# Performance work log

Measured on AMD Instinct MI355X. Metric: run time of the kernel, lower is better.

The kernel has to match this reference:

```python
import jax, jax.numpy as jnp
import numpy as np

D = 1024
H = 16
HD = D // H
T = 2048
B = 2
EPS = 1e-7

def setup_inputs() -> dict:
    key = jax.random.key(0)
    ks = jax.random.split(key, 16)
    s = 0.02
    return {
        "x":  jax.random.normal(ks[0], (B, T, D), jnp.float32),
        "Wq": jax.random.normal(ks[1], (D, D), jnp.float32) * s,
        "bq": jnp.zeros((D,), jnp.float32),
        "Wk": jax.random.normal(ks[2], (D, D), jnp.float32) * s,
        "bk": jnp.zeros((D,), jnp.float32),
        "Wv": jax.random.normal(ks[3], (D, D), jnp.float32) * s,
        "bv": jnp.zeros((D,), jnp.float32),
        "Wo": jax.random.normal(ks[4], (D, D), jnp.float32) * s,
        "bo": jnp.zeros((D,), jnp.float32),
        "W1": jax.random.normal(ks[5], (D, 4 * D), jnp.float32) * s,
        "b1": jnp.zeros((4 * D,), jnp.float32),
        "W2": jax.random.normal(ks[6], (4 * D, D), jnp.float32) * s,
        "b2": jnp.zeros((D,), jnp.float32),
        "g1": jnp.ones((D,), jnp.float32),
        "be1": jnp.zeros((D,), jnp.float32),
        "g2": jnp.ones((D,), jnp.float32),
        "be2": jnp.zeros((D,), jnp.float32),
    }

def layer_norm(x, gamma, beta):
    mu = jnp.mean(x, axis=-1, keepdims=True)
    var = jnp.mean(jnp.square(x - mu), axis=-1, keepdims=True)  # biased var
    return (x - mu) / jnp.sqrt(var + EPS) * gamma + beta

def attention(x, Wq, bq, Wk, bk, Wv, bv, Wo, bo):
    b, t, d = x.shape
    q = (x @ Wq + bq).reshape(b, t, H, HD).transpose(0, 2, 1, 3)  # [B,H,T,HD]
    k = (x @ Wk + bk).reshape(b, t, H, HD).transpose(0, 2, 1, 3)
    v = (x @ Wv + bv).reshape(b, t, H, HD).transpose(0, 2, 1, 3)
    scores = jnp.einsum("bhqd,bhkd->bhqk", q, k) / np.sqrt(HD).astype(np.float32)
    causal = jnp.tril(jnp.ones((t, t), bool))
    scores = jnp.where(causal, scores, -jnp.inf)
    attn = jax.nn.softmax(scores, axis=-1)
    out = jnp.einsum("bhqk,bhkd->bhqd", attn, v)
    out = out.transpose(0, 2, 1, 3).reshape(b, t, d)
    return out @ Wo + bo

def reference(x, Wq, bq, Wk, bk, Wv, bv, Wo, bo, W1, b1, W2, b2, g1, be1, g2, be2):
    x = x + attention(layer_norm(x, g1, be1), Wq, bq, Wk, bk, Wv, bv, Wo, bo)
    h = layer_norm(x, g2, be2)
    x = x + (jax.nn.relu(h @ W1 + b1) @ W2 + b2)
    return x
```

## Files before the change

### kernel.cpp

```cpp
#include <hip/hip_runtime.h>
#include <hip/hip_bf16.h>

#define Dm 1024
#define Hn 16
#define HDm 64
#define Tm 2048
#define Bm 2
#define MR (Bm*Tm)
#define SQK 3072

typedef __attribute__((ext_vector_type(8))) short bfrag8;
typedef __attribute__((ext_vector_type(4))) float floatx4;

__device__ __forceinline__ float bf2f(ushort u){
  union { unsigned int i; float f; } c; c.i = ((unsigned int)u)<<16; return c.f;
}
__device__ __forceinline__ ushort f2bf(float f){
  unsigned int u = __float_as_uint(f);
  u += 0x7fffu + ((u>>16)&1u);
  return (ushort)(u>>16);
}
__device__ __forceinline__ void gl2lds16(const ushort* g, ushort* l){
  __builtin_amdgcn_global_load_lds(
    (const __attribute__((address_space(1))) unsigned int*)g,
    (__attribute__((address_space(3))) unsigned int*)l,
    16, 0, 0);
}
__device__ __forceinline__ int is_f32(const unsigned int* g1w){
  return *g1w == 0x3F800000u;
}

__global__ __launch_bounds__(256) void prep_vec(const void* bq, const void* bk, const void* bv,
                                                const void* bo, const void* b1, const void* b2,
                                                const void* g1, const void* be1,
                                                const void* g2, const void* be2,
                                                float* __restrict__ dst){
  int i = blockIdx.x*256 + threadIdx.x;
  if (i >= 13312) return;
  int f = is_f32((const unsigned int*)g1);
  const void* src; int off;
  if      (i < 1024)  { src = bq;  off = i; }
  else if (i < 2048)  { src = bk;  off = i-1024; }
  else if (i < 3072)  { src = bv;  off = i-2048; }
  else if (i < 4096)  { src = bo;  off = i-3072; }
  else if (i < 8192)  { src = b1;  off = i-4096; }
  else if (i < 9216)  { src = b2;  off = i-8192; }
  else if (i < 10240) { src = g1;  off = i-9216; }
  else if (i < 11264) { src = be1; off = i-10240; }
  else if (i < 12288) { src = g2;  off = i-11264; }
  else                { src = be2; off = i-12288; }
  dst[i] = f ? ((const float*)src)[off] : bf2f(((const ushort*)src)[off]);
}

__device__ __forceinline__ void transpose_body(const void* src, ushort* dst,
                                               int K, int N, int f32){
  __shared__ ushort s[32][33];
  int bx = blockIdx.x, by = blockIdx.y;
  int tx = threadIdx.x, ty = threadIdx.y;
#pragma unroll
  for(int r=0;r<4;r++){
    size_t gi = (size_t)(by*32+ty+8*r)*N + bx*32+tx;
    s[ty+8*r][tx] = f32 ? f2bf(((const float*)src)[gi]) : ((const ushort*)src)[gi];
  }
  __syncthreads();
#pragma unroll
  for(int r=0;r<4;r++)
    dst[(size_t)(bx*32+ty+8*r)*K + by*32+tx] = s[tx][ty+8*r];
}
__global__ __launch_bounds__(256) void transpose_cast(const void* __restrict__ src,
                                                      ushort* __restrict__ dst,
                                                      int K, int N, const unsigned int* g1w){
  transpose_body(src, dst, K, N, is_f32(g1w));
}
__global__ __launch_bounds__(256) void transpose_qkvo(const void* Wq, const void* Wk,
                                                      const void* Wv, const void* Wo,
                                                      ushort* __restrict__ Wqkvt,
                                                      ushort* __restrict__ Wot,
                                                      const unsigned int* g1w){
  int z = blockIdx.z;
  const void* src = (z==0)?Wq:(z==1)?Wk:(z==2)?Wv:Wo;
  ushort* dst = (z<3) ? (Wqkvt + (size_t)z*1024*1024) : Wot;
  transpose_body(src, dst, 1024, 1024, is_f32(g1w));
}

__global__ __launch_bounds__(256) void vtrans(const ushort* __restrict__ qkv,
                                              ushort* __restrict__ vt){
  __shared__ ushort s[32][33];
  int bhz = blockIdx.z;
  int bx = blockIdx.x;
  int by = blockIdx.y;
  int tx = threadIdx.x, ty = threadIdx.y;
  int b = bhz>>4, h = bhz&15;
  const ushort* src = qkv + (size_t)b*Tm*SQK + 2048 + h*64;
#pragma unroll
  for(int r=0;r<4;r++)
    s[ty+8*r][tx] = src[(size_t)(bx*32+ty+8*r)*SQK + by*32+tx];
  __syncthreads();
  ushort* dst = vt + (size_t)bhz*HDm*Tm;
#pragma unroll
  for(int r=0;r<4;r++)
    dst[(size_t)(by*32+ty+8*r)*Tm + bx*32+tx] = s[tx][ty+8*r];
}

template<int MODE>
__global__ __launch_bounds__(256) void ln_kernel(const void* __restrict__ xin,
                                                 const float* __restrict__ g,
                                                 const float* __restrict__ be,
                                                 ushort* __restrict__ out,
                                                 const unsigned int* g1w){
  int row = blockIdx.x;
  int tid = threadIdx.x;
  size_t base = (size_t)row*Dm + tid*4;
  float v[4];
  bool f32in = (MODE==1) || (MODE==0 && is_f32(g1w));
  if (f32in){
    const float4 t = *(const float4*)((const float*)xin + base);
    v[0]=t.x; v[1]=t.y; v[2]=t.z; v[3]=t.w;
  } else {
    ushort4 t = *(const ushort4*)((const ushort*)xin + base);
    v[0]=bf2f(t.x); v[1]=bf2f(t.y); v[2]=bf2f(t.z); v[3]=bf2f(t.w);
  }
  float s  = v[0]+v[1]+v[2]+v[3];
  float s2 = v[0]*v[0]+v[1]*v[1]+v[2]*v[2]+v[3]*v[3];
#pragma unroll
  for(int o=1;o<64;o<<=1){
    s  += __shfl_xor(s,  o, 64);
    s2 += __shfl_xor(s2, o, 64);
  }
  __shared__ float red[8];
  int wv = tid>>6;
  if ((tid&63)==0){ red[wv]=s; red[wv+4]=s2; }
  __syncthreads();
  s  = red[0]+red[1]+red[2]+red[3];
  s2 = red[4]+red[5]+red[6]+red[7];
  float mu  = s  * (1.0f/Dm);
  float var = s2 * (1.0f/Dm) - mu*mu;
  float rstd = rsqrtf(var + 1e-7f);
  float4 gg = *(const float4*)(g  + tid*4);
  float4 bb = *(const float4*)(be + tid*4);
  ushort4 o4;
  o4.x = f2bf((v[0]-mu)*rstd*gg.x+bb.x);
  o4.y = f2bf((v[1]-mu)*rstd*gg.y+bb.y);
  o4.z = f2bf((v[2]-mu)*rstd*gg.z+bb.z);
  o4.w = f2bf((v[3]-mu)*rstd*gg.w+bb.w);
  *(ushort4*)(out + base) = o4;
}

#define BKt 64
enum { E_BF16=0, E_RELU=1, E_OPROJ=2, E_FINALB=3, E_PARTB=4 };

template<int EPI>
__global__ __launch_bounds__(256) void gemm_bt(const ushort* __restrict__ A, int lda,
                                               const ushort* __restrict__ Bt, int ldb,
                                               const float* __restrict__ bias,
                                               void* __restrict__ Cout, int ldc,
                                               int Ki,
                                               const unsigned int* g1w){
  __shared__ ushort As[128*BKt];
  __shared__ ushort Bs[128*BKt];
  int tid = threadIdx.x;
  int bn = blockIdx.x, bm = blockIdx.y;
  int wv = tid>>6, lane = tid&63;
  int quad = lane>>4, l16 = lane&15;
  int wm = (wv&1)*64, wn = (wv>>1)*64;
  floatx4 acc[4][4] = {};
  int koff = (EPI==E_PARTB) ? blockIdx.z*Ki : 0;
  const ushort* Aptr = A  + (size_t)bm*128*lda + koff;
  const ushort* Bptr = Bt + (size_t)bn*128*ldb + koff;
  int rl = lane>>3;
  int cs = ((lane&7) ^ rl)*8;

  for(int k0=0; k0<Ki; k0+=BKt){
    __syncthreads();
#pragma unroll
    for(int c=0;c<4;c++){
      gl2lds16(&Aptr[(size_t)(wv*32 + c*8 + rl)*lda + k0 + cs], &As[(wv*32 + c*8)*BKt]);
      gl2lds16(&Bptr[(size_t)(wv*32 + c*8 + rl)*ldb + k0 + cs], &Bs[(wv*32 + c*8)*BKt]);
    }
    __syncthreads();
#pragma unroll
    for(int f=0;f<2;f++){
      int sw = (((f<<2)|quad) ^ (l16&7))*8;
      bfrag8 a[4], b[4];
#pragma unroll
      for(int i=0;i<4;i++) a[i] = *(const bfrag8*)&As[(wm+i*16+l16)*BKt + sw];
#pragma unroll
      for(int j=0;j<4;j++) b[j] = *(const bfrag8*)&Bs[(wn+j*16+l16)*BKt + sw];
#pragma unroll
      for(int i=0;i<4;i++)
#pragma unroll
        for(int j=0;j<4;j++)
          acc[i][j] = __builtin_amdgcn_mfma_f32_16x16x32_bf16(a[i], b[j], acc[i][j], 0,0,0);
    }
  }

  ushort* part = (EPI==E_PARTB) ? ((ushort*)Cout + (size_t)blockIdx.z*MR*1024) : (ushort*)Cout;
#pragma unroll
  for(int i=0;i<4;i++){
    int gr = bm*128 + wm + i*16 + quad*4;
#pragma unroll
    for(int j=0;j<4;j++){
      int gc = bn*128 + wn + j*16 + l16;
      float bb = (EPI==E_PARTB) ? 0.0f : bias[gc];
#pragma unroll
      for(int rg=0; rg<4; rg++){
        size_t idx = (size_t)(gr+rg)*ldc + gc;
        float val = acc[i][j][rg] + bb;
        if (EPI==E_BF16)        part[idx] = f2bf(val);
        else if (EPI==E_RELU)   part[idx] = f2bf(val>0.0f?val:0.0f);
        else       part[idx] = f2bf(val);
      }
    }
  }
}

__global__ __launch_bounds__(256) void ffn2_reduce(const ushort* __restrict__ p0,
                                                   const ushort* __restrict__ p1,
                                                   const float* __restrict__ bias,
                                                   const ushort* __restrict__ resid,
                                                   void* __restrict__ out,
                                                   const unsigned int* g1w){
  int e = (blockIdx.x*256 + threadIdx.x)*4;
  ushort4 a = *(const ushort4*)&p0[e];
  ushort4 b = *(const ushort4*)&p1[e];
  ushort4 r = *(const ushort4*)&resid[e];
  float4 bb = *(const float4*)&bias[e & 1023];
  float v0 = bf2f(a.x)+bf2f(b.x)+bb.x+bf2f(r.x);
  float v1 = bf2f(a.y)+bf2f(b.y)+bb.y+bf2f(r.y);
  float v2 = bf2f(a.z)+bf2f(b.z)+bb.z+bf2f(r.z);
  float v3 = bf2f(a.w)+bf2f(b.w)+bb.w+bf2f(r.w);
  if (is_f32(g1w)){
    float4 o = {v0,v1,v2,v3};
    *(float4*)((float*)out + e) = o;
  } else {
    ushort4 o = {f2bf(v0),f2bf(v1),f2bf(v2),f2bf(v3)};
    *(ushort4*)((ushort*)out + e) = o;
  }
}

template<int EPI>
__global__ __launch_bounds__(128) void gemm64_bt(const ushort* __restrict__ A, int lda,
                                                 const ushort* __restrict__ Bt, int ldb,
                                                 const float* __restrict__ bias,
                                                 const void*   __restrict__ resid,
                                                 void* __restrict__ Cout, int ldc,
                                                 int Ki,
                                                 const unsigned int* g1w){
  __shared__ ushort As[64*BKt];
  __shared__ ushort Bs[64*BKt];
  int tid = threadIdx.x;
  int id = blockIdx.x;
  int xcd = id&7, sdec = id>>3;
  int bn = sdec&15, bm = (sdec>>4)*8 + xcd;
  int wv = tid>>6, lane = tid&63;
  int quad = lane>>4, l16 = lane&15;
  int wm = wv*32;
  floatx4 acc[2][4] = {};
  const ushort* Aptr = A  + (size_t)bm*64*lda;
  const ushort* Bptr = Bt + (size_t)bn*64*ldb;
  int rl = lane>>3;
  int cs = ((lane&7) ^ rl)*8;

  for(int k0=0; k0<Ki; k0+=BKt){
    __syncthreads();
#pragma unroll
    for(int c=0;c<4;c++){
      gl2lds16(&Aptr[(size_t)(wv*32 + c*8 + rl)*lda + k0 + cs], &As[(wv*32 + c*8)*BKt]);
      gl2lds16(&Bptr[(size_t)(wv*32 + c*8 + rl)*ldb + k0 + cs], &Bs[(wv*32 + c*8)*BKt]);
    }
    __syncthreads();
#pragma unroll
    for(int f=0;f<2;f++){
      int sw = (((f<<2)|quad) ^ (l16&7))*8;
      bfrag8 a[2], b[4];
#pragma unroll
      for(int i=0;i<2;i++) a[i] = *(const bfrag8*)&As[(wm+i*16+l16)*BKt + sw];
#pragma unroll
      for(int j=0;j<4;j++) b[j] = *(const bfrag8*)&Bs[(j*16+l16)*BKt + sw];
#pragma unroll
      for(int i=0;i<2;i++)
#pragma unroll
        for(int j=0;j<4;j++)
          acc[i][j] = __builtin_amdgcn_mfma_f32_16x16x32_bf16(a[i], b[j], acc[i][j], 0,0,0);
    }
  }

  int f32 = is_f32(g1w);
#pragma unroll
  for(int i=0;i<2;i++){
    int gr = bm*64 + wm + i*16 + quad*4;
#pragma unroll
    for(int j=0;j<4;j++){
      int gc = bn*64 + j*16 + l16;
      float bb = bias[gc];
#pragma unroll
      for(int rg=0; rg<4; rg++){
        size_t idx = (size_t)(gr+rg)*ldc + gc;
        float val = acc[i][j][rg] + bb;
        if (EPI==E_OPROJ){
          float r = f32 ? ((const float*)resid)[idx] : bf2f(((const ushort*)resid)[idx]);
          ((ushort*)Cout)[idx] = f2bf(val + r);
        } else {
          float r = bf2f(((const ushort*)resid)[idx]);
          if (f32) ((float*)Cout)[idx] = val + r;
          else     ((ushort*)Cout)[idx] = f2bf(val + r);
        }
      }
    }
  }
}

#define PSTR2 136

__global__ __launch_bounds__(256) void attn_mfma(const ushort* __restrict__ qkv,
                                                 const ushort* __restrict__ vt,
                                                 ushort* __restrict__ out){
  __shared__ ushort Ks[128*64];
  __shared__ ushort Vs[64*128];
  __shared__ ushort Ps[64*PSTR2];
  int id = blockIdx.x;
  int xcd = id&7, sdec = id>>3;
  int bxp = sdec&15, hb = sdec>>4;
  int h = xcd + 8*(hb&1), b = hb>>1;
  int tid = threadIdx.x;
  int wv = tid>>6, lane = tid&63;
  int quad = lane>>4, l16 = lane&15;
  const ushort* qbase = qkv + (size_t)b*Tm*SQK + h*HDm;
  const ushort* kbase = qbase + Dm;
  const ushort* vtb   = vt + (size_t)(b*Hn+h)*HDm*Tm;
  size_t obase = (size_t)b*Tm*Dm + (size_t)h*HDm;
  int rl = lane>>3;
  int cs = ((lane&7) ^ rl)*8;
  int vrow = lane>>4;
  int l7 = l16 & 7;

  for(int half=0; half<2; half++){
    int qt = half ? (31 - bxp) : bxp;
    int qrow = qt*64 + wv*16 + l16;
    bfrag8 aq[2];
#pragma unroll
    for(int f=0;f<2;f++){
      bfrag8 raw = *(const bfrag8*)&qbase[(size_t)qrow*SQK + f*32 + quad*8];
#pragma unroll
      for(int e=0;e<8;e++) aq[f][e] = (short)f2bf(bf2f((ushort)raw[e])*0.125f);
    }

    floatx4 oacc[4] = {};
    float lacc[4] = {0.0f,0.0f,0.0f,0.0f};
    int qabs0 = qt*64 + wv*16 + quad*4;
    int nr = (qt+2)>>1;

    for(int r=0; r<nr; r++){
      __syncthreads();
#pragma unroll
      for(int c=0;c<4;c++){
        int kr0 = wv*32 + c*8;
        gl2lds16(&kbase[(size_t)(r*128 + kr0 + rl)*SQK + cs], &Ks[kr0*64]);
        int d0 = wv*16 + c*4;
        int drow = d0 + vrow;
        int gg = (lane&15) ^ (drow&7);
        gl2lds16(&vtb[(size_t)drow*Tm + r*128 + gg*8], &Vs[d0*128]);
      }
      __syncthreads();

      floatx4 s[8];
#pragma unroll
      for(int j=0;j<8;j++){
        int kr = j*16 + l16;
        int k7 = kr & 7;
        bfrag8 b0 = *(const bfrag8*)&Ks[kr*64 + ((quad     ^ k7)*8)];
        bfrag8 b1 = *(const bfrag8*)&Ks[kr*64 + (((4|quad) ^ k7)*8)];
        floatx4 z = {0.0f,0.0f,0.0f,0.0f};
        z = __builtin_amdgcn_mfma_f32_16x16x32_bf16(aq[0], b0, z, 0,0,0);
        z = __builtin_amdgcn_mfma_f32_16x16x32_bf16(aq[1], b1, z, 0,0,0);
        s[j] = z;
      }
      if (2*r+1 >= qt){
#pragma unroll
        for(int j=0;j<8;j++){
          int gk = r*128 + j*16 + l16;
#pragma unroll
          for(int rg=0;rg<4;rg++)
            if (gk > qabs0 + rg) s[j][rg] = -1.0e30f;
        }
      }

#pragma unroll
      for(int j=0;j<8;j++)
#pragma unroll
        for(int rg=0;rg<4;rg++){
          float p = __expf(s[j][rg]);
          lacc[rg] += p;
          Ps[(wv*16 + quad*4+rg)*PSTR2 + j*16 + l16] = f2bf(p);
        }

      bfrag8 ap[4];
#pragma unroll
      for(int c=0;c<4;c++)
        ap[c] = *(const bfrag8*)&Ps[(wv*16 + l16)*PSTR2 + (c*4+quad)*8];
#pragma unroll
      for(int j=0;j<4;j++){
        int dr = j*16 + l16;
        int d7 = dr & 7;
#pragma unroll
        for(int c=0;c<4;c++){
          bfrag8 bv = *(const bfrag8*)&Vs[dr*128 + (((c*4+quad) ^ d7)*8)];
          oacc[j] = __builtin_amdgcn_mfma_f32_16x16x32_bf16(ap[c], bv, oacc[j], 0,0,0);
        }
      }
    }

#pragma unroll
    for(int o=1;o<16;o<<=1)
#pragma unroll
      for(int rg=0;rg<4;rg++) lacc[rg] += __shfl_xor(lacc[rg], o, 64);
    float inv[4];
#pragma unroll
    for(int rg=0;rg<4;rg++) inv[rg] = 1.0f / lacc[rg];

#pragma unroll
    for(int j=0;j<4;j++)
#pragma unroll
      for(int rg=0;rg<4;rg++){
        int t = qt*64 + wv*16 + quad*4 + rg;
        out[obase + (size_t)t*Dm + j*16 + l16] = f2bf(oacc[j][rg] * inv[rg]);
      }
  }
}

extern "C" void kernel_launch(void* const* d_in, const int* in_sizes, int n_in,
                              void* d_out, int out_size, void* d_ws, size_t ws_size,
                              hipStream_t stream) {
  const void* x   = d_in[0];
  const void* Wq  = d_in[1];
  const void* bq  = d_in[2];
  const void* Wk  = d_in[3];
  const void* bk  = d_in[4];
  const void* Wv  = d_in[5];
  const void* bv  = d_in[6];
  const void* Wo  = d_in[7];
  const void* bo  = d_in[8];
  const void* W1  = d_in[9];
  const void* b1  = d_in[10];
  const void* W2  = d_in[11];
  const void* b2  = d_in[12];
  const void* g1  = d_in[13];
  const void* be1 = d_in[14];
  const void* g2  = d_in[15];
  const void* be2 = d_in[16];
  const unsigned int* g1w = (const unsigned int*)g1;

  char* ws = (char*)d_ws;
  const size_t MB = 1024*1024;
  float*  biasf = (float*)(ws + 65536);
  ushort* Wqkvt = (ushort*)(ws + 1*MB);
  ushort* Wot   = (ushort*)(ws + 7*MB);
  ushort* W1t   = (ushort*)(ws + 9*MB);
  ushort* W2t   = (ushort*)(ws + 17*MB);
  ushort* p0    = (ushort*)(ws + 1*MB);
  ushort* p1    = (ushort*)(ws + 9*MB);
  ushort* ln1   = (ushort*)(ws + 25*MB);
  ushort* vtb   = (ushort*)(ws + 25*MB);
  ushort* h2    = (ushort*)(ws + 25*MB);
  ushort* qkv   = (ushort*)(ws + 33*MB);
  ushort* atb   = (ushort*)(ws + 57*MB);
  ushort* x1b   = (ushort*)(ws + 65*MB);
  ushort* h1    = (ushort*)(ws + 33*MB);

  prep_vec<<<52, 256, 0, stream>>>(bq,bk,bv,bo,b1,b2,g1,be1,g2,be2, biasf);

  dim3 tb(32,8);
  transpose_qkvo<<<dim3(32,32,4), tb, 0, stream>>>(Wq, Wk, Wv, Wo, Wqkvt, Wot, g1w);
  transpose_cast<<<dim3(128,32), tb, 0, stream>>>(W1, W1t, 1024, 4096, g1w);
  transpose_cast<<<dim3(32,128), tb, 0, stream>>>(W2, W2t, 4096, 1024, g1w);

  ln_kernel<0><<<MR, 256, 0, stream>>>(x, biasf+9216, biasf+10240, ln1, g1w);

  gemm_bt<E_BF16><<<dim3(24,32), 256, 0, stream>>>(ln1, 1024, Wqkvt, 1024, biasf, qkv, SQK, 1024, g1w);

  vtrans<<<dim3(64,2,32), tb, 0, stream>>>(qkv, vtb);

  attn_mfma<<<512, 256, 0, stream>>>(qkv, vtb, atb);

  gemm64_bt<E_OPROJ><<<1024, 128, 0, stream>>>(atb, 1024, Wot, 1024, biasf+3072, x, x1b, 1024, 1024, g1w);

  ln_kernel<2><<<MR, 256, 0, stream>>>(x1b, biasf+11264, biasf+12288, h2, g1w);

  gemm_bt<E_RELU><<<dim3(32,32), 256, 0, stream>>>(h2, 1024, W1t, 1024, biasf+4096, h1, 4096, 1024, g1w);
  gemm_bt<E_PARTB><<<dim3(8,32,2), 256, 0, stream>>>(h1, 4096, W2t, 4096, nullptr, p0, 1024, 2048, g1w);
  ffn2_reduce<<<4096, 256, 0, stream>>>(p0, p1, biasf+8192, x1b, d_out, g1w);
}
```

Before: 362.3 us.

## Remap GEMM blocks across XCDs and use 4-way split-K for FFN2

Remaps block indices in the QKV, FFN1 and FFN2 GEMMs so that blocks landing on the same XCD share A/B tiles, which should improve L2 locality on the chiplet layout. Adds a 4-way split-K variant of the FFN2 GEMM, writing partials into workspace offsets, with a 4-input reduce kernel, to raise block count (1024 vs 512) and so occupancy. The cost is extra partial traffic in the reduce. It falls back to the old path when the workspace is too small.

```diff
diff --git a/kernel.cpp b/kernel.cpp
--- a/kernel.cpp
+++ b/kernel.cpp
@@ -29,6 +29,11 @@
 __device__ __forceinline__ int is_f32(const unsigned int* g1w){
   return *g1w == 0x3F800000u;
 }
+
+#define POFF0 (1ul*524288)
+#define POFF1 (9ul*524288)
+#define POFF2 (25ul*524288)
+#define POFF3 (73ul*524288)
 
 __global__ __launch_bounds__(256) void prep_vec(const void* bq, const void* bk, const void* bv,
                                                 const void* bo, const void* b1, const void* b2,
@@ -147,7 +152,7 @@
 }
 
 #define BKt 64
-enum { E_BF16=0, E_RELU=1, E_OPROJ=2, E_FINALB=3, E_PARTB=4 };
+enum { E_BF16=0, E_RELU=1, E_OPROJ=2, E_FINALB=3, E_PARTB=4, E_PARTB4=5 };
 
 template<int EPI>
 __global__ __launch_bounds__(256) void gemm_bt(const ushort* __restrict__ A, int lda,
@@ -159,12 +164,31 @@
   __shared__ ushort As[128*BKt];
   __shared__ ushort Bs[128*BKt];
   int tid = threadIdx.x;
-  int bn = blockIdx.x, bm = blockIdx.y;
+  int bn, bm, zid = 0;
+  if (EPI==E_BF16){
+    int lin = blockIdx.y*24 + blockIdx.x;
+    int xcd = lin&7, pos = lin>>3;
+    bn = (xcd&1)*12 + pos%12;
+    bm = (xcd>>1)*8 + pos/12;
+  } else if (EPI==E_RELU){
+    int lin = blockIdx.y*32 + blockIdx.x;
+    int xcd = lin&7, pos = lin>>3;
+    bm = (xcd&3)*8 + (pos&7);
+    bn = (xcd>>2)*16 + (pos>>3);
+  } else if (EPI==E_PARTB4){
+    int lin = (blockIdx.z*32 + blockIdx.y)*8 + blockIdx.x;
+    int xcd = lin&7, pos = lin>>3;
+    zid = xcd>>1;
+    bm = (xcd&1)*16 + (pos>>3);
+    bn = pos&7;
+  } else {
+    bn = blockIdx.x; bm = blockIdx.y; zid = blockIdx.z;
+  }
   int wv = tid>>6, lane = tid&63;
   int quad = lane>>4, l16 = lane&15;
   int wm = (wv&1)*64, wn = (wv>>1)*64;
   floatx4 acc[4][4] = {};
-  int koff = (EPI==E_PARTB) ? blockIdx.z*Ki : 0;
+  int koff = (EPI==E_PARTB || EPI==E_PARTB4) ? zid*Ki : 0;
   const ushort* Aptr = A  + (size_t)bm*128*lda + koff;
   const ushort* Bptr = Bt + (size_t)bn*128*ldb + koff;
   int rl = lane>>3;
@@ -194,21 +218,22 @@
     }
   }
 
-  ushort* part = (EPI==E_PARTB) ? ((ushort*)Cout + (size_t)blockIdx.z*MR*1024) : (ushort*)Cout;
+  ushort* part = (ushort*)Cout;
+  if (EPI==E_PARTB)  part += (size_t)zid*MR*1024;
+  if (EPI==E_PARTB4) part += (zid==0?POFF0 : zid==1?POFF1 : zid==2?POFF2 : POFF3);
 #pragma unroll
   for(int i=0;i<4;i++){
     int gr = bm*128 + wm + i*16 + quad*4;
 #pragma unroll
     for(int j=0;j<4;j++){
       int gc = bn*128 + wn + j*16 + l16;
-      float bb = (EPI==E_PARTB) ? 0.0f : bias[gc];
+      float bb = (EPI==E_PARTB || EPI==E_PARTB4) ? 0.0f : bias[gc];
 #pragma unroll
       for(int rg=0; rg<4; rg++){
         size_t idx = (size_t)(gr+rg)*ldc + gc;
         float val = acc[i][j][rg] + bb;
-        if (EPI==E_BF16)        part[idx] = f2bf(val);
-        else if (EPI==E_RELU)   part[idx] = f2bf(val>0.0f?val:0.0f);
-        else       part[idx] = f2bf(val);
+        if (EPI==E_RELU)   part[idx] = f2bf(val>0.0f?val:0.0f);
+        else               part[idx] = f2bf(val);
       }
     }
   }
@@ -229,6 +254,31 @@
   float v1 = bf2f(a.y)+bf2f(b.y)+bb.y+bf2f(r.y);
   float v2 = bf2f(a.z)+bf2f(b.z)+bb.z+bf2f(r.z);
   float v3 = bf2f(a.w)+bf2f(b.w)+bb.w+bf2f(r.w);
+  if (is_f32(g1w)){
+    float4 o = {v0,v1,v2,v3};
+    *(float4*)((float*)out + e) = o;
+  } else {
+    ushort4 o = {f2bf(v0),f2bf(v1),f2bf(v2),f2bf(v3)};
+    *(ushort4*)((ushort*)out + e) = o;
+  }
+}
+
+__global__ __launch_bounds__(256) void ffn2_reduce4(const ushort* __restrict__ pb,
+                                                    const float* __restrict__ bias,
+                                                    const ushort* __restrict__ resid,
+                                                    void* __restrict__ out,
+                                                    const unsigned int* g1w){
+  int e = (blockIdx.x*256 + threadIdx.x)*4;
+  ushort4 a = *(const ushort4*)&pb[POFF0 + e];
+  ushort4 b = *(const ushort4*)&pb[POFF1 + e];
+  ushort4 c = *(const ushort4*)&pb[POFF2 + e];
+  ushort4 d = *(const ushort4*)&pb[POFF3 + e];
+  ushort4 r = *(const ushort4*)&resid[e];
+  float4 bb = *(const float4*)&bias[e & 1023];
+  float v0 = bf2f(a.x)+bf2f(b.x)+bf2f(c.x)+bf2f(d.x)+bb.x+bf2f(r.x);
+  float v1 = bf2f(a.y)+bf2f(b.y)+bf2f(c.y)+bf2f(d.y)+bb.y+bf2f(r.y);
+  float v2 = bf2f(a.z)+bf2f(b.z)+bf2f(c.z)+bf2f(d.z)+bb.z+bf2f(r.z);
+  float v3 = bf2f(a.w)+bf2f(b.w)+bf2f(c.w)+bf2f(d.w)+bb.w+bf2f(r.w);
   if (is_f32(g1w)){
     float4 o = {v0,v1,v2,v3};
     *(float4*)((float*)out + e) = o;
@@ -487,6 +537,12 @@
   ln_kernel<2><<<MR, 256, 0, stream>>>(x1b, biasf+11264, biasf+12288, h2, g1w);
 
   gemm_bt<E_RELU><<<dim3(32,32), 256, 0, stream>>>(h2, 1024, W1t, 1024, biasf+4096, h1, 4096, 1024, g1w);
-  gemm_bt<E_PARTB><<<dim3(8,32,2), 256, 0, stream>>>(h1, 4096, W2t, 4096, nullptr, p0, 1024, 2048, g1w);
-  ffn2_reduce<<<4096, 256, 0, stream>>>(p0, p1, biasf+8192, x1b, d_out, g1w);
-}
+
+  if (ws_size >= 82*MB){
+    gemm_bt<E_PARTB4><<<dim3(8,32,4), 256, 0, stream>>>(h1, 4096, W2t, 4096, nullptr, d_ws, 1024, 1024, g1w);
+    ffn2_reduce4<<<4096, 256, 0, stream>>>((const ushort*)d_ws, biasf+8192, x1b, d_out, g1w);
+  } else {
+    gemm_bt<E_PARTB><<<dim3(8,32,2), 256, 0, stream>>>(h1, 4096, W2t, 4096, nullptr, p0, 1024, 2048, g1w);
+    ffn2_reduce<<<4096, 256, 0, stream>>>(p0, p1, biasf+8192, x1b, d_out, g1w);
+  }
+}
```

Measured after the change: 361.2 us. No clear change (-0.3%).
